# Kernel optimization log

Hardware: AMD Instinct MI355X
Metric: run time of the kernel (lower is better)

The kernel has to match this reference:

```python
import jax, jax.numpy as jnp
import numpy as np

G = 8            # grid_size
G2 = G * G       # total_grid_size = 64
NS = 2.0         # neighborhood_size
H = 64           # h_dim
A = 1024         # bottleneck_dim == attention_dim
S = 32           # number of sequences
N = 64           # pedestrians per sequence
P = 4096         # scene boundary points per sequence (down_samples)
B = S * N        # total batch = 2048


def setup_inputs() -> dict:
    key = jax.random.key(0)
    ks = jax.random.split(key, 16)
    starts = jnp.arange(S, dtype=jnp.int32) * N
    seq_start_end = jnp.stack([starts, starts + N], axis=1)  # (S, 2) uniform groups
    return {
        "h_states": jax.random.normal(ks[0], (1, B, H), jnp.float32),
        "end_pos": jax.random.normal(ks[1], (B, 2), jnp.float32),
        "rel_pos": jax.random.normal(ks[2], (B, 2), jnp.float32) * 0.1,
        "scene_info": jax.random.normal(ks[3], (S, P, 2), jnp.float32),
        # Attention_Decoder params (soft attention over G2 grid cells, encoder_dim=1)
        "W_enc": jax.random.normal(ks[4], (1, A), jnp.float32) * 0.05,
        "b_enc": jnp.zeros((A,), jnp.float32),
        "W_dec": jax.random.normal(ks[5], (H, A), jnp.float32) * 0.05,
        "b_dec": jnp.zeros((A,), jnp.float32),
        "w_full": jax.random.normal(ks[6], (A, 1), jnp.float32) * 0.05,
        "b_full": jnp.zeros((1,), jnp.float32),
        "W_out": jax.random.normal(ks[7], (1 + H + 4, A), jnp.float32) * 0.05,  # [ctx, h, embed_info]
        "b_out": jnp.zeros((A,), jnp.float32),
        # mlp_pool: Linear(A, A) + BatchNorm1d + ReLU
        "W_mlp": jax.random.normal(ks[8], (A, A), jnp.float32) * 0.05,
        "b_mlp": jnp.zeros((A,), jnp.float32),
        "gamma": jnp.ones((A,), jnp.float32),
        "beta": jnp.zeros((A,), jnp.float32),
        "seq_start_end": seq_start_end,
    }


def _occupancy(end_pos, scene_info, num_seqs, peds, grid_size, ns):
    """Vectorized per-pedestrian grid-cell binning + scatter-add occupancy.
    end_pos: (num_seqs*peds, 2), scene_info: (num_seqs, P, 2) -> (B, G2)."""
    g2 = grid_size * grid_size
    b = num_seqs * peds
    ep = end_pos.reshape(num_seqs, peds, 1, 2)
    sx = scene_info[:, None, :, 0]  # (S, 1, P)
    sy = scene_info[:, None, :, 1]
    tl_x = ep[..., 0] - ns / 2
    tl_y = ep[..., 1] + ns / 2
    br_x = ep[..., 0] + ns / 2
    br_y = ep[..., 1] - ns / 2
    cell_x = jnp.floor((sx - tl_x) / ns * grid_size)   # (S, N, P)
    cell_y = jnp.floor((tl_y - sy) / ns * grid_size)
    cell = (cell_x + cell_y * grid_size).astype(jnp.int32)
    # point is out-of-bound if outside the ped's neighborhood box (matches torch mask)
    oob = (sx >= br_x) | (sx <= tl_x) | (sy >= tl_y) | (sy <= br_y)
    ped = jnp.arange(b, dtype=jnp.int32).reshape(num_seqs, peds, 1)
    # torch scatters masked points into slot 0 then drops it; we use one dump slot at the end
    idx = jnp.where(oob, b * g2, ped * g2 + cell)      # (S, N, P)
    counts = jax.ops.segment_sum(
        jnp.ones(idx.size, jnp.float32), idx.reshape(-1), num_segments=b * g2 + 1)
    return counts[:-1].reshape(b, g2)


def reference(h_states, end_pos, rel_pos, scene_info,
              W_enc, b_enc, W_dec, b_dec, w_full, b_full,
              W_out, b_out, W_mlp, b_mlp, gamma, beta, seq_start_end):
    num_seqs = seq_start_end.shape[0]
    b = end_pos.shape[0]
    peds = b // num_seqs
    occ = _occupancy(end_pos, scene_info, num_seqs, peds, G, NS)   # (B, G2)
    enc = occ[..., None]                                           # (B, G2, 1)
    h = h_states.reshape(b, -1)                                    # (B, H)
    embed_info = jnp.concatenate([end_pos, rel_pos], axis=1)       # (B, 4)
    # soft attention over the G2 grid cells conditioned on the decoder hidden state
    att = jax.nn.relu(enc @ W_enc + b_enc + (h @ W_dec + b_dec)[:, None, :])  # (B, G2, A)
    e = (att @ w_full)[..., 0] + b_full                            # (B, G2)
    alpha = jax.nn.softmax(e, axis=1)
    ctx = jnp.sum(alpha[..., None] * enc, axis=1)                  # (B, 1)
    pool = jnp.concatenate([ctx, h, embed_info], axis=1) @ W_out + b_out  # (B, A)
    # mlp_pool: Linear -> BatchNorm1d (training stats, biased var) -> ReLU
    y = pool @ W_mlp + b_mlp
    mu = jnp.mean(y, axis=0)
    var = jnp.mean((y - mu) ** 2, axis=0)
    y = gamma * (y - mu) * jax.lax.rsqrt(var + 1e-5) + beta
    return jax.nn.relu(y)
```

## Files before the change

### kernel.cpp

```cpp
#include <hip/hip_runtime.h>
#include <hip/hip_bf16.h>


#define NG2  64
#define NPTS 4096

typedef unsigned short ushort_t;
typedef __attribute__((ext_vector_type(8))) short bf16x8;
typedef __attribute__((ext_vector_type(4))) float f32x4;

struct PrepPtrs { const void* p[16]; };

__device__ __forceinline__ float bf2f(ushort_t u) {
  return __uint_as_float(((unsigned int)u) << 16);
}
__device__ __forceinline__ ushort_t f2bf(float f) {
  __hip_bfloat16 b = __float2bfloat16(f);
  return *reinterpret_cast<ushort_t*>(&b);
}
__device__ __forceinline__ float lde(const void* p, size_t i, int fl) {
  return fl ? bf2f(((const ushort_t*)p)[i]) : ((const float*)p)[i];
}
__device__ __forceinline__ int block_flag(const ushort_t* h) {
  __shared__ int bad_sh;
  if (threadIdx.x == 0) bad_sh = 0;
  __syncthreads();
  float v = bf2f(h[threadIdx.x & 255]);
  if (!(fabsf(v) <= 1e4f)) atomicOr(&bad_sh, 1);
  __syncthreads();
  return (bad_sh == 0) ? 1 : 0;
}

__device__ __forceinline__ void tp_body(const void* in, int fl, int job,
                                        int Kin, int Kpad, ushort_t* out) {
  __shared__ ushort_t t[32][40];
  int n0 = (job & 31) * 32, k0 = (job >> 5) * 32;
  int r = threadIdx.x >> 3, c4 = (threadIdx.x & 7) * 4;
  ushort4 v = make_ushort4(0, 0, 0, 0);
  if (k0 + r < Kin) {
    size_t off = (size_t)(k0 + r) * 1024 + n0 + c4;
    if (fl) {
      v = *(const ushort4*)((const ushort_t*)in + off);
    } else {
      float4 f = *(const float4*)((const float*)in + off);
      v = make_ushort4(f2bf(f.x), f2bf(f.y), f2bf(f.z), f2bf(f.w));
    }
  }
  *(ushort4*)(&t[r][c4]) = v;
  __syncthreads();
  int n = threadIdx.x >> 3, kk = (threadIdx.x & 7) * 4;
  ushort4 o = make_ushort4(t[kk][n], t[kk + 1][n], t[kk + 2][n], t[kk + 3][n]);
  *(ushort4*)(out + (size_t)(n0 + n) * Kpad + k0 + kk) = o;
}

__global__ __launch_bounds__(256) void k_prep(PrepPtrs ptrs,
                                              float* __restrict__ conv,
                                              ushort_t* __restrict__ hbf,
                                              ushort_t* __restrict__ WdecT,
                                              ushort_t* __restrict__ WoutT,
                                              ushort_t* __restrict__ WmlpT,
                                              ushort_t* __restrict__ Xcat0,
                                              float* __restrict__ occ,
                                              float* __restrict__ stats) {
  int b = blockIdx.x;
  int fl = block_flag((const ushort_t*)ptrs.p[0]);
  if (b < 9) {
    int idx = (b * 256 + threadIdx.x) * 4;
    int seg = idx >> 10, off = idx & 1023;
    float4 o;
    if (fl) {
      const unsigned int* src = (const unsigned int*)ptrs.p[7 + seg];
      uint2 u = *(const uint2*)(src + (off >> 1));
      o.x = __uint_as_float((u.x & 0xFFFFu) << 16);
      o.y = __uint_as_float(u.x & 0xFFFF0000u);
      o.z = __uint_as_float((u.y & 0xFFFFu) << 16);
      o.w = __uint_as_float(u.y & 0xFFFF0000u);
    } else {
      o = *(const float4*)((const float*)ptrs.p[7 + seg] + off);
    }
    *(float4*)(conv + idx) = o;
  } else if (b < 73) {
    int i = (b - 9) * 256 + threadIdx.x;
    if (fl) {
      ((uint4*)hbf)[i] = ((const uint4*)ptrs.p[0])[i];
    } else {
      float4 f0 = ((const float4*)ptrs.p[0])[2 * i];
      float4 f1 = ((const float4*)ptrs.p[0])[2 * i + 1];
      ((ushort4*)hbf)[2 * i]     = make_ushort4(f2bf(f0.x), f2bf(f0.y), f2bf(f0.z), f2bf(f0.w));
      ((ushort4*)hbf)[2 * i + 1] = make_ushort4(f2bf(f1.x), f2bf(f1.y), f2bf(f1.z), f2bf(f1.w));
    }
  } else if (b < 137) {
    tp_body(ptrs.p[1], fl, b - 73, 64, 64, WdecT);
  } else if (b < 233) {
    const void* wout1 = fl ? (const void*)((const ushort_t*)ptrs.p[2] + 1024)
                           : (const void*)((const float*)ptrs.p[2] + 1024);
    tp_body(wout1, fl, b - 137, 68, 96, WoutT);
  } else if (b < 489) {
    __shared__ ushort_t t64[64 * 68];
    int job = b - 233;
    int n0 = (job & 15) * 64, k0 = (job >> 4) * 64;
    const void* in = ptrs.p[3];
#pragma unroll
    for (int i = 0; i < 4; i++) {
      int chunk = threadIdx.x + i * 256;
      int r = chunk >> 4, c4 = (chunk & 15) * 4;
      ushort4 v;
      size_t off = (size_t)(k0 + r) * 1024 + n0 + c4;
      if (fl) {
        v = *(const ushort4*)((const ushort_t*)in + off);
      } else {
        float4 f = *(const float4*)((const float*)in + off);
        v = make_ushort4(f2bf(f.x), f2bf(f.y), f2bf(f.z), f2bf(f.w));
      }
      *(ushort4*)(&t64[r * 68 + c4]) = v;
    }
    __syncthreads();
#pragma unroll
    for (int i = 0; i < 4; i++) {
      int chunk = threadIdx.x + i * 256;
      int n = chunk >> 4, k4 = (chunk & 15) * 4;
      ushort4 o = make_ushort4(t64[(k4 + 0) * 68 + n], t64[(k4 + 1) * 68 + n],
                               t64[(k4 + 2) * 68 + n], t64[(k4 + 3) * 68 + n]);
      *(ushort4*)(WmlpT + (size_t)(n0 + n) * 1024 + k0 + k4) = o;
    }
  } else if (b < 681) {
    int flat = (b - 489) * 256 + threadIdx.x;
    int e4 = flat * 4;
    int r = e4 / 96, c = e4 - r * 96;
    ushort4 v = make_ushort4(0, 0, 0, 0);
    if (c < 64) {
      if (fl) v = *(const ushort4*)((const ushort_t*)ptrs.p[0] + r * 64 + c);
      else {
        float4 f = *(const float4*)((const float*)ptrs.p[0] + r * 64 + c);
        v = make_ushort4(f2bf(f.x), f2bf(f.y), f2bf(f.z), f2bf(f.w));
      }
    } else if (c == 64) {
      v.x = f2bf(lde(ptrs.p[4], 2 * r, fl));
      v.y = f2bf(lde(ptrs.p[4], 2 * r + 1, fl));
      v.z = f2bf(lde(ptrs.p[5], 2 * r, fl));
      v.w = f2bf(lde(ptrs.p[5], 2 * r + 1, fl));
    }
    *(ushort4*)(Xcat0 + e4) = v;
  } else if (b < 1193) {
    int wave = threadIdx.x >> 6, lane = threadIdx.x & 63;
    int i = (b - 681) * 4 + wave;
    int s = i >> 6;
    __shared__ float cnth[4][NG2];
    cnth[wave][lane] = 0.0f;
    __syncthreads();
    float ex = lde(ptrs.p[4], 2 * i, fl), ey = lde(ptrs.p[4], 2 * i + 1, fl);
    float tlx = ex - 1.0f, tly = ey + 1.0f, brx = ex + 1.0f, bry = ey - 1.0f;
    const void* scn = ptrs.p[6];
    for (int p = lane; p < NPTS; p += 64) {
      size_t pi = (size_t)s * NPTS + p;
      float sx, sy;
      if (fl) {
        unsigned int u = ((const unsigned int*)scn)[pi];
        sx = __uint_as_float((u & 0xFFFFu) << 16);
        sy = __uint_as_float(u & 0xFFFF0000u);
      } else {
        float2 f = *((const float2*)scn + pi);
        sx = f.x; sy = f.y;
      }
      bool oob = (sx >= brx) || (sx <= tlx) || (sy >= tly) || (sy <= bry);
      if (!oob) {
        int cx = (int)floorf((sx - tlx) * 0.5f * 8.0f);
        int cy = (int)floorf((tly - sy) * 0.5f * 8.0f);
        int cell = cx + cy * 8;
        if (cell >= 0 && cell < NG2) atomicAdd(&cnth[wave][cell], 1.0f);
      }
    }
    __syncthreads();
    occ[(size_t)i * NG2 + lane] = cnth[wave][lane];
  } else {
#pragma unroll
    for (int k = 0; k < 8; k++) stats[threadIdx.x + 256 * k] = 0.0f;
  }
}

template <int K, int EPI>
__device__ __forceinline__ void mgemm_body(
    ushort_t* As, ushort_t* Bs, int m0, int n0,
    const ushort_t* __restrict__ A, int lda,
    const ushort_t* __restrict__ BT, int ldb,
    const float* __restrict__ bias1, const float* __restrict__ bias2,
    ushort_t* __restrict__ outb, float* __restrict__ outf) {
  int tid = threadIdx.x;
  int wave = tid >> 6, lane = tid & 63, l15 = lane & 15, kg = lane >> 4;
  f32x4 acc[4][2] = {};
  int ar = tid >> 2, ag = tid & 3;
  int aswz = ag ^ ((ar >> 1) & 3);
  for (int k0 = 0; k0 < K; k0 += 32) {
    uint4 av = *(const uint4*)(A + (size_t)(m0 + ar) * lda + k0 + ag * 8);
    *(uint4*)(&As[ar * 32 + aswz * 8]) = av;
#pragma unroll
    for (int i = 0; i < 2; i++) {
      int c = tid + i * 256;
      int br = c >> 2, bg = c & 3;
      int bswz = bg ^ ((br >> 1) & 3);
      uint4 bv = *(const uint4*)(BT + (size_t)(n0 + br) * ldb + k0 + bg * 8);
      *(uint4*)(&Bs[br * 32 + bswz * 8]) = bv;
    }
    __syncthreads();
    bf16x8 af[4], bfr[2];
#pragma unroll
    for (int mt = 0; mt < 4; mt++) {
      int row = mt * 16 + l15;
      int swz = kg ^ ((row >> 1) & 3);
      af[mt] = *(const bf16x8*)(&As[row * 32 + swz * 8]);
    }
#pragma unroll
    for (int nt = 0; nt < 2; nt++) {
      int row = wave * 32 + nt * 16 + l15;
      int swz = kg ^ ((row >> 1) & 3);
      bfr[nt] = *(const bf16x8*)(&Bs[row * 32 + swz * 8]);
    }
#pragma unroll
    for (int mt = 0; mt < 4; mt++)
#pragma unroll
      for (int nt = 0; nt < 2; nt++)
        acc[mt][nt] = __builtin_amdgcn_mfma_f32_16x16x32_bf16(af[mt], bfr[nt], acc[mt][nt], 0, 0, 0);
    __syncthreads();
  }
#pragma unroll
  for (int nt = 0; nt < 2; nt++) {
    int col = n0 + wave * 32 + nt * 16 + l15;
    float bsum = (EPI == 0) ? (bias1[col] + bias2[col]) : bias1[col];
#pragma unroll
    for (int mt = 0; mt < 4; mt++) {
#pragma unroll
      for (int r = 0; r < 4; r++) {
        int rowm = m0 + mt * 16 + kg * 4 + r;
        float v = acc[mt][nt][r] + bsum;
        if (EPI == 3) outf[(size_t)rowm * 1024 + col] = v;
        else outb[(size_t)rowm * 1024 + col] = f2bf(v);
      }
    }
  }
}

__global__ __launch_bounds__(256) void k_gemm2(
    const ushort_t* __restrict__ hbf, const ushort_t* __restrict__ WdecT,
    const float* __restrict__ benc, const float* __restrict__ bdec,
    ushort_t* __restrict__ hd_out,
    const ushort_t* __restrict__ Xcat0, const ushort_t* __restrict__ WoutT,
    const float* __restrict__ bout, float* __restrict__ P1) {
  __shared__ ushort_t As[64 * 32];
  __shared__ ushort_t Bs[128 * 32];
  int m0 = blockIdx.x * 64, n0 = blockIdx.y * 128;
  if (blockIdx.z == 0)
    mgemm_body<64, 0>(As, Bs, m0, n0, hbf, 64, WdecT, 64, benc, bdec, hd_out, nullptr);
  else
    mgemm_body<96, 3>(As, Bs, m0, n0, Xcat0, 96, WoutT, 96, bout, nullptr, nullptr, P1);
}

__global__ __launch_bounds__(256) void k_ygemm(
    const ushort_t* __restrict__ A, const ushort_t* __restrict__ BT,
    const float* __restrict__ bias1, ushort_t* __restrict__ outb,
    float* __restrict__ stats) {
  __shared__ ushort_t As[64 * 32];
  __shared__ ushort_t Bs[64 * 32];
  int m0 = blockIdx.x * 64, n0 = blockIdx.y * 64;
  int tid = threadIdx.x;
  int wave = tid >> 6, lane = tid & 63, l15 = lane & 15, kg = lane >> 4;
  f32x4 acc[4] = {};
  int ar = tid >> 2, ag = tid & 3;
  int aswz = ag ^ ((ar >> 1) & 3);
  for (int k0 = 0; k0 < 1024; k0 += 32) {
    uint4 av = *(const uint4*)(A + (size_t)(m0 + ar) * 1024 + k0 + ag * 8);
    *(uint4*)(&As[ar * 32 + aswz * 8]) = av;
    {
      int br = tid >> 2, bg = tid & 3;
      int bswz = bg ^ ((br >> 1) & 3);
      uint4 bv = *(const uint4*)(BT + (size_t)(n0 + br) * 1024 + k0 + bg * 8);
      *(uint4*)(&Bs[br * 32 + bswz * 8]) = bv;
    }
    __syncthreads();
    bf16x8 af[4], bfr;
#pragma unroll
    for (int mt = 0; mt < 4; mt++) {
      int row = mt * 16 + l15;
      int swz = kg ^ ((row >> 1) & 3);
      af[mt] = *(const bf16x8*)(&As[row * 32 + swz * 8]);
    }
    {
      int row = wave * 16 + l15;
      int swz = kg ^ ((row >> 1) & 3);
      bfr = *(const bf16x8*)(&Bs[row * 32 + swz * 8]);
    }
#pragma unroll
    for (int mt = 0; mt < 4; mt++)
      acc[mt] = __builtin_amdgcn_mfma_f32_16x16x32_bf16(af[mt], bfr, acc[mt], 0, 0, 0);
    __syncthreads();
  }
  int col = n0 + wave * 16 + l15;
  float bsum = bias1[col];
  float s1 = 0.0f, s2 = 0.0f;
#pragma unroll
  for (int mt = 0; mt < 4; mt++) {
#pragma unroll
    for (int r = 0; r < 4; r++) {
      int rowm = m0 + mt * 16 + kg * 4 + r;
      float v = acc[mt][r] + bsum;
      outb[(size_t)rowm * 1024 + col] = f2bf(v);
      s1 += v; s2 = fmaf(v, v, s2);
    }
  }
  s1 += __shfl_down(s1, 16); s2 += __shfl_down(s2, 16);
  s1 += __shfl_down(s1, 32); s2 += __shfl_down(s2, 32);
  if (lane < 16) {
    atomicAdd(&stats[col], s1);
    atomicAdd(&stats[1024 + col], s2);
  }
}

__global__ __launch_bounds__(256) void k_ectx(
    const float* __restrict__ occ,
    const float* __restrict__ Wenc, const float* __restrict__ wfull,
    const float* __restrict__ w0, const float* __restrict__ P1,
    const ushort_t* __restrict__ hd, ushort_t* __restrict__ pool) {
  int wave = threadIdx.x >> 6, lane = threadIdx.x & 63;
  int p = blockIdx.x * 4 + wave;
  __shared__ float occ_sh[4][64];
  occ_sh[wave][lane] = occ[p * 64 + lane];
  float hdv[16], we[16], wf[16];
#pragma unroll
  for (int j = 0; j < 16; j++) {
    int a = lane + j * 64;
    hdv[j] = bf2f(hd[(size_t)p * 1024 + a]);
    we[j] = Wenc[a];
    wf[j] = wfull[a];
  }
  float e_mine = 0.0f;
  for (int g = 0; g < 64; g++) {
    float c = occ_sh[wave][g];
    float s = 0.0f;
#pragma unroll
    for (int j = 0; j < 16; j++)
      s += fmaxf(fmaf(c, we[j], hdv[j]), 0.0f) * wf[j];
#pragma unroll
    for (int off = 32; off > 0; off >>= 1) s += __shfl_xor(s, off);
    if (lane == g) e_mine = s;
  }
  float m = e_mine;
#pragma unroll
  for (int off = 32; off > 0; off >>= 1) m = fmaxf(m, __shfl_xor(m, off));
  float xe = __expf(e_mine - m);
  float den = xe;
#pragma unroll
  for (int off = 32; off > 0; off >>= 1) den += __shfl_xor(den, off);
  float cp = xe * occ_sh[wave][lane];
#pragma unroll
  for (int off = 32; off > 0; off >>= 1) cp += __shfl_xor(cp, off);
  float ctx = cp / den;
#pragma unroll
  for (int j = 0; j < 16; j++) {
    int a = lane + j * 64;
    pool[(size_t)p * 1024 + a] = f2bf(fmaf(ctx, w0[a], P1[(size_t)p * 1024 + a]));
  }
}

__global__ void k_norm(const ushort_t* __restrict__ y_mf,
                       const float* __restrict__ stats,
                       const float* __restrict__ gamma, const float* __restrict__ beta,
                       const ushort_t* __restrict__ hsrc, void* __restrict__ out) {
  int fl = block_flag(hsrc);
  int idx = (blockIdx.x * 256 + threadIdx.x) * 4;
  int col = idx & 1023;
  float vv[4];
#pragma unroll
  for (int j = 0; j < 4; j++) vv[j] = bf2f(y_mf[idx + j]);
  float4 s1 = *(const float4*)(stats + col);
  float4 s2 = *(const float4*)(stats + 1024 + col);
  float4 gm = *(const float4*)(gamma + col);
  float4 bt = *(const float4*)(beta + col);
  const float ib = 1.0f / 2048.0f;
  float m1[4] = {s1.x, s1.y, s1.z, s1.w};
  float m2[4] = {s2.x, s2.y, s2.z, s2.w};
  float gg[4] = {gm.x, gm.y, gm.z, gm.w};
  float bb[4] = {bt.x, bt.y, bt.z, bt.w};
  float o[4];
#pragma unroll
  for (int j = 0; j < 4; j++) {
    float mu = m1[j] * ib;
    float var = fmaf(-mu, mu, m2[j] * ib);
    o[j] = fmaxf(fmaf(gg[j] * (vv[j] - mu), rsqrtf(var + 1e-5f), bb[j]), 0.0f);
  }
  if (fl) {
    ushort4 ov = make_ushort4(f2bf(o[0]), f2bf(o[1]), f2bf(o[2]), f2bf(o[3]));
    *(ushort4*)((ushort_t*)out + idx) = ov;
  } else {
    *(float4*)((float*)out + idx) = make_float4(o[0], o[1], o[2], o[3]);
  }
}

extern "C" void kernel_launch(void* const* d_in, const int* in_sizes, int n_in,
                              void* d_out, int out_size, void* d_ws, size_t ws_size,
                              hipStream_t stream) {
  float* ws = (float*)d_ws;
  float* conv   = ws;
  float* c_Wenc = conv + 0;
  float* c_benc = conv + 1024;
  float* c_bdec = conv + 2048;
  float* c_wful = conv + 3072;
  float* c_bout = conv + 4096;
  float* c_bmlp = conv + 5120;
  float* c_gam  = conv + 6144;
  float* c_bet  = conv + 7168;
  float* c_w0   = conv + 8192;
  float* occ    = ws + 9216;
  float* stats  = ws + 140288;
  float* P1     = ws + 142336;
  ushort_t* u0    = (ushort_t*)(ws + 2239488);
  ushort_t* hbf   = u0;
  ushort_t* WdecT = u0 + 131072;
  ushort_t* WoutT = u0 + 196608;
  ushort_t* WmlpT = u0 + 294912;
  ushort_t* Xcat0 = u0 + 1343488;
  ushort_t* y_mf  = u0 + 1540096;
  ushort_t* hd_bf   = (ushort_t*)d_out;
  ushort_t* pool_mf = (ushort_t*)d_out;

  PrepPtrs ptrs;
  ptrs.p[0] = d_in[0];
  ptrs.p[1] = d_in[6];
  ptrs.p[2] = d_in[10];
  ptrs.p[3] = d_in[12];
  ptrs.p[4] = d_in[1];
  ptrs.p[5] = d_in[2];
  ptrs.p[6] = d_in[3];
  ptrs.p[7]  = d_in[4];
  ptrs.p[8]  = d_in[5];
  ptrs.p[9]  = d_in[7];
  ptrs.p[10] = d_in[8];
  ptrs.p[11] = d_in[11];
  ptrs.p[12] = d_in[13];
  ptrs.p[13] = d_in[14];
  ptrs.p[14] = d_in[15];
  ptrs.p[15] = d_in[10];

  k_prep<<<1194, 256, 0, stream>>>(ptrs, conv, hbf, WdecT, WoutT, WmlpT,
                                   Xcat0, occ, stats);

  k_gemm2<<<dim3(32, 8, 2), 256, 0, stream>>>(hbf, WdecT, c_benc, c_bdec, hd_bf,
                                              Xcat0, WoutT, c_bout, P1);

  k_ectx<<<512, 256, 0, stream>>>(occ, c_Wenc, c_wful, c_w0, P1, hd_bf, pool_mf);

  k_ygemm<<<dim3(32, 16), 256, 0, stream>>>(pool_mf, WmlpT, c_bmlp, y_mf, stats);

  k_norm<<<2048, 256, 0, stream>>>(y_mf, stats, c_gam, c_bet,
                                   (const ushort_t*)d_in[0], d_out);
}
```

Measured before the change: 167.4 us.

## Parallelize occupancy per block and restructure attention scores via shared memory

The occupancy binning now assigns one pedestrian per 256-thread block instead of one per wave, so each block scans the scene points with four times as many threads, and the prep launch grows to match. The attention-score kernel stages Wenc, w_full and the decoder row in shared memory. Each lane then computes one grid cell's score with a serial loop over the 1024 attention dims, which replaces the per-cell 64-lane shuffle reductions. This removes many cross-lane reductions, at the cost of 20 KB of shared memory per block and a longer serial per-lane loop.

```diff
diff --git a/kernel.cpp b/kernel.cpp
--- a/kernel.cpp
+++ b/kernel.cpp
@@ -141,17 +141,16 @@
       v.w = f2bf(lde(ptrs.p[5], 2 * r + 1, fl));
     }
     *(ushort4*)(Xcat0 + e4) = v;
-  } else if (b < 1193) {
-    int wave = threadIdx.x >> 6, lane = threadIdx.x & 63;
-    int i = (b - 681) * 4 + wave;
+  } else if (b < 2729) {
+    int i = b - 681;
     int s = i >> 6;
-    __shared__ float cnth[4][NG2];
-    cnth[wave][lane] = 0.0f;
+    __shared__ float cnth[NG2];
+    if (threadIdx.x < NG2) cnth[threadIdx.x] = 0.0f;
     __syncthreads();
     float ex = lde(ptrs.p[4], 2 * i, fl), ey = lde(ptrs.p[4], 2 * i + 1, fl);
     float tlx = ex - 1.0f, tly = ey + 1.0f, brx = ex + 1.0f, bry = ey - 1.0f;
     const void* scn = ptrs.p[6];
-    for (int p = lane; p < NPTS; p += 64) {
+    for (int p = threadIdx.x; p < NPTS; p += 256) {
       size_t pi = (size_t)s * NPTS + p;
       float sx, sy;
       if (fl) {
@@ -167,11 +166,11 @@
         int cx = (int)floorf((sx - tlx) * 0.5f * 8.0f);
         int cy = (int)floorf((tly - sy) * 0.5f * 8.0f);
         int cell = cx + cy * 8;
-        if (cell >= 0 && cell < NG2) atomicAdd(&cnth[wave][cell], 1.0f);
+        if (cell >= 0 && cell < NG2) atomicAdd(&cnth[cell], 1.0f);
       }
     }
     __syncthreads();
-    occ[(size_t)i * NG2 + lane] = cnth[wave][lane];
+    if (threadIdx.x < NG2) occ[i * NG2 + threadIdx.x] = cnth[threadIdx.x];
   } else {
 #pragma unroll
     for (int k = 0; k < 8; k++) stats[threadIdx.x + 256 * k] = 0.0f;
@@ -319,29 +318,44 @@
     const float* __restrict__ Wenc, const float* __restrict__ wfull,
     const float* __restrict__ w0, const float* __restrict__ P1,
     const ushort_t* __restrict__ hd, ushort_t* __restrict__ pool) {
+  __shared__ float we_sh[1024];
+  __shared__ float wf_sh[1024];
+  __shared__ float hd_sh[4][1024];
+  __shared__ float occ_sh[4][64];
   int wave = threadIdx.x >> 6, lane = threadIdx.x & 63;
   int p = blockIdx.x * 4 + wave;
-  __shared__ float occ_sh[4][64];
+  {
+    int t = threadIdx.x * 4;
+    *(float4*)&we_sh[t] = *(const float4*)(Wenc + t);
+    *(float4*)&wf_sh[t] = *(const float4*)(wfull + t);
+  }
   occ_sh[wave][lane] = occ[p * 64 + lane];
-  float hdv[16], we[16], wf[16];
-#pragma unroll
-  for (int j = 0; j < 16; j++) {
-    int a = lane + j * 64;
-    hdv[j] = bf2f(hd[(size_t)p * 1024 + a]);
-    we[j] = Wenc[a];
-    wf[j] = wfull[a];
-  }
-  float e_mine = 0.0f;
-  for (int g = 0; g < 64; g++) {
-    float c = occ_sh[wave][g];
-    float s = 0.0f;
-#pragma unroll
-    for (int j = 0; j < 16; j++)
-      s += fmaxf(fmaf(c, we[j], hdv[j]), 0.0f) * wf[j];
-#pragma unroll
-    for (int off = 32; off > 0; off >>= 1) s += __shfl_xor(s, off);
-    if (lane == g) e_mine = s;
-  }
+  {
+    const ushort_t* hrow = hd + (size_t)p * 1024;
+#pragma unroll
+    for (int j = 0; j < 4; j++) {
+      int a = lane * 4 + j * 256;
+      ushort4 v = *(const ushort4*)(hrow + a);
+      hd_sh[wave][a + 0] = bf2f(v.x);
+      hd_sh[wave][a + 1] = bf2f(v.y);
+      hd_sh[wave][a + 2] = bf2f(v.z);
+      hd_sh[wave][a + 3] = bf2f(v.w);
+    }
+  }
+  __syncthreads();
+  float c = occ_sh[wave][lane];
+  float s0 = 0.0f, s1 = 0.0f, s2 = 0.0f, s3 = 0.0f;
+#pragma unroll 4
+  for (int a = 0; a < 1024; a += 4) {
+    float4 we4 = *(const float4*)&we_sh[a];
+    float4 hd4 = *(const float4*)&hd_sh[wave][a];
+    float4 wf4 = *(const float4*)&wf_sh[a];
+    s0 += fmaxf(fmaf(c, we4.x, hd4.x), 0.0f) * wf4.x;
+    s1 += fmaxf(fmaf(c, we4.y, hd4.y), 0.0f) * wf4.y;
+    s2 += fmaxf(fmaf(c, we4.z, hd4.z), 0.0f) * wf4.z;
+    s3 += fmaxf(fmaf(c, we4.w, hd4.w), 0.0f) * wf4.w;
+  }
+  float e_mine = (s0 + s1) + (s2 + s3);
   float m = e_mine;
 #pragma unroll
   for (int off = 32; off > 0; off >>= 1) m = fmaxf(m, __shfl_xor(m, off));
@@ -349,7 +363,7 @@
   float den = xe;
 #pragma unroll
   for (int off = 32; off > 0; off >>= 1) den += __shfl_xor(den, off);
-  float cp = xe * occ_sh[wave][lane];
+  float cp = xe * c;
 #pragma unroll
   for (int off = 32; off > 0; off >>= 1) cp += __shfl_xor(cp, off);
   float ctx = cp / den;
@@ -439,7 +453,7 @@
   ptrs.p[14] = d_in[15];
   ptrs.p[15] = d_in[10];
 
-  k_prep<<<1194, 256, 0, stream>>>(ptrs, conv, hbf, WdecT, WoutT, WmlpT,
+  k_prep<<<2730, 256, 0, stream>>>(ptrs, conv, hbf, WdecT, WoutT, WmlpT,
                                    Xcat0, occ, stats);
 
   k_gemm2<<<dim3(32, 8, 2), 256, 0, stream>>>(hbf, WdecT, c_benc, c_bdec, hd_bf,
```

Result: faster. 155.4 us (-7.2%).
